# Optimization experiments

Hardware: AMD Instinct MI355X
Metric: run time of the kernel (lower is better)

## Reference

```python
import jax, jax.numpy as jnp
import numpy as np

N_HEADS = 16
EMBED = 1024
SEQ = 2048
BATCH = 4
GELU_C = 0.044715
EPS = 1e-5


def gelu_tanh(x):
    return 0.5 * x * (1.0 + jnp.tanh(jnp.sqrt(2.0 / jnp.pi) * (x + GELU_C * x ** 3)))


def layer_norm(x, scale, shift):
    mean = jnp.mean(x, axis=-1, keepdims=True)
    var = jnp.var(x, axis=-1, keepdims=True)
    return scale * (x - mean) / jnp.sqrt(var + EPS) + shift


def setup_inputs() -> dict:
    key = jax.random.key(0)
    ks = jax.random.split(key, 8)
    d = EMBED
    s = 0.02
    return {
        "X": jax.random.normal(ks[0], (BATCH, SEQ, d), dtype=jnp.float32),
        "Wq": jax.random.normal(ks[1], (d, d), dtype=jnp.float32) * s,
        "Wk": jax.random.normal(ks[2], (d, d), dtype=jnp.float32) * s,
        "Wv": jax.random.normal(ks[3], (d, d), dtype=jnp.float32) * s,
        "Wo": jax.random.normal(ks[4], (d, d), dtype=jnp.float32) * s,
        "W1": jax.random.normal(ks[5], (d, 4 * d), dtype=jnp.float32) * s,
        "b1": jnp.zeros((4 * d,), dtype=jnp.float32),
        "W2": jax.random.normal(ks[6], (4 * d, d), dtype=jnp.float32) * s,
        "b2": jnp.zeros((d,), dtype=jnp.float32),
        "ln1_scale": jnp.ones((d,), dtype=jnp.float32),
        "ln1_shift": jnp.zeros((d,), dtype=jnp.float32),
        "ln2_scale": jnp.ones((d,), dtype=jnp.float32),
        "ln2_shift": jnp.zeros((d,), dtype=jnp.float32),
    }


def attention(x, Wq, Wk, Wv, Wo):
    b, s, d = x.shape
    h, dh = N_HEADS, d // N_HEADS
    q = (x @ Wq).reshape(b, s, h, dh).transpose(0, 2, 1, 3)  # [b,h,s,dh]
    k = (x @ Wk).reshape(b, s, h, dh).transpose(0, 2, 1, 3)
    v = (x @ Wv).reshape(b, s, h, dh).transpose(0, 2, 1, 3)
    scores = jnp.einsum("bhqd,bhkd->bhqk", q, k) / jnp.sqrt(jnp.float32(dh))
    causal = jnp.tril(jnp.ones((s, s), dtype=bool))
    scores = jnp.where(causal, scores, -jnp.inf)
    w = jax.nn.softmax(scores, axis=-1)  # dropout rate 0 -> identity
    ctx = jnp.einsum("bhqk,bhkd->bhqd", w, v)
    ctx = ctx.transpose(0, 2, 1, 3).reshape(b, s, d)
    return ctx @ Wo


def reference(X, Wq, Wk, Wv, Wo, W1, b1, W2, b2,
              ln1_scale, ln1_shift, ln2_scale, ln2_shift):
    h = layer_norm(X, ln1_scale, ln1_shift)
    X = X + attention(h, Wq, Wk, Wv, Wo)
    h = layer_norm(X, ln2_scale, ln2_shift)
    h = gelu_tanh(h @ W1 + b1) @ W2 + b2
    return X + h
```

## Files before the change

### kernel.cpp

```cpp
#include <hip/hip_runtime.h>

typedef unsigned short u16;
typedef __attribute__((ext_vector_type(8))) short bf16x8;
typedef __attribute__((ext_vector_type(4))) float fx4;

#define MFMA16(a, b, c) __builtin_amdgcn_mfma_f32_16x16x32_bf16((a), (b), (c), 0, 0, 0)

__device__ __forceinline__ u16 f2bf(float f) {
  unsigned u = __float_as_uint(f);
  u += 0x7fffu + ((u >> 16) & 1u);
  return (u16)(u >> 16);
}

__device__ __forceinline__ void gload_lds16(const void* g, void* l) {
  __builtin_amdgcn_global_load_lds((const __attribute__((address_space(1))) void*)g,
                                   (__attribute__((address_space(3))) void*)l,
                                   16, 0, 0);
}

struct WP {
  const float* s[6];
  u16* d[6];
};
__global__ __launch_bounds__(256) void tcvt_all(WP p) {
  __shared__ float t[32][33];
  const int id = blockIdx.x;
  int which, bx, by, R, C;
  if (id < 4096) {
    which = id >> 10;
    const int q = id & 1023;
    bx = q >> 5; by = q & 31; R = 1024; C = 1024;
  } else if (id < 8192) {
    which = 4;
    const int q = id - 4096;
    bx = q & 127; by = q >> 7; R = 1024; C = 4096;
  } else {
    which = 5;
    const int q = id - 8192;
    bx = q & 31; by = q >> 5; R = 4096; C = 1024;
  }
  const float* src = p.s[which];
  u16* dst = p.d[which];
  const int tx = threadIdx.x & 31, ty = threadIdx.x >> 5;
#pragma unroll
  for (int i = 0; i < 4; ++i)
    t[ty + i * 8][tx] = src[(size_t)(by * 32 + ty + i * 8) * C + bx * 32 + tx];
  __syncthreads();
#pragma unroll
  for (int i = 0; i < 4; ++i)
    dst[(size_t)(bx * 32 + ty + i * 8) * R + by * 32 + tx] = f2bf(t[tx][ty + i * 8]);
}

__global__ __launch_bounds__(256) void ln_kernel(const float* __restrict__ x,
                                                 const float* __restrict__ sc,
                                                 const float* __restrict__ sh,
                                                 u16* __restrict__ out) {
  const int row = blockIdx.x, tid = threadIdx.x;
  const float4 v = ((const float4*)(x + (size_t)row * 1024))[tid];
  float s = v.x + v.y + v.z + v.w;
  float ss = v.x * v.x + v.y * v.y + v.z * v.z + v.w * v.w;
#pragma unroll
  for (int d = 32; d >= 1; d >>= 1) {
    s += __shfl_xor(s, d);
    ss += __shfl_xor(ss, d);
  }
  __shared__ float rs[4], rq[4];
  const int w = tid >> 6;
  if ((tid & 63) == 0) { rs[w] = s; rq[w] = ss; }
  __syncthreads();
  s = rs[0] + rs[1] + rs[2] + rs[3];
  ss = rq[0] + rq[1] + rq[2] + rq[3];
  const float mean = s * (1.f / 1024.f);
  const float var = ss * (1.f / 1024.f) - mean * mean;
  const float rstd = rsqrtf(var + 1e-5f);
  const float4 g = ((const float4*)sc)[tid];
  const float4 b = ((const float4*)sh)[tid];
  ushort4 o;
  o.x = f2bf(g.x * (v.x - mean) * rstd + b.x);
  o.y = f2bf(g.y * (v.y - mean) * rstd + b.y);
  o.z = f2bf(g.z * (v.z - mean) * rstd + b.z);
  o.w = f2bf(g.w * (v.w - mean) * rstd + b.w);
  ((ushort4*)(out + (size_t)row * 1024))[tid] = o;
}

__device__ __forceinline__ void xcd_map(int bid, int NTN, int& tMi, int& tNi) {
  const int xcd = bid & 7, i = bid >> 3;
  tMi = xcd + 8 * (i / NTN);
  tNi = i % NTN;
}

template <int MODE, int BN>
__global__ __launch_bounds__(512, 1) void gemm8p(
    const u16* __restrict__ A, const u16* __restrict__ Bt, int K, int NTN,
    void* __restrict__ outp, const float* __restrict__ aux,
    u16* __restrict__ qd, u16* __restrict__ kd, u16* __restrict__ vd) {
  constexpr int WN = (BN == 256) ? 4 : 2;
  constexpr int WM = 8 / WN;
  constexpr int MR = 256 / (16 * WM);
  constexpr int MR2 = MR / 2;
  constexpr int BLOADS = BN / 128;
  __shared__ u16 lA[2][2][256 * 32];
  __shared__ u16 lB[2][2][BN * 32];
  const int tid = threadIdx.x;
  const int lane = tid & 63, w = tid >> 6;
  const int lo = lane & 15, hi = lane >> 4;
  const int wm = w / WN, wn = w % WN;
  int tMi, tNi;
  xcd_map(blockIdx.x, NTN, tMi, tNi);
  const int tM = tMi * 256, tN = tNi * BN;
  const int NT = K >> 6;
  const int NIT = K >> 7;

#define STG_A(TI, KSH, GK)                                                       \
  do {                                                                           \
    _Pragma("unroll") for (int j = 0; j < 2; ++j) {                              \
      const int idx = j * 512 + tid;                                             \
      const int row = idx >> 2, u = idx & 3;                                     \
      gload_lds16(A + (size_t)(tM + row) * K + (GK) + ((u ^ ((row >> 1) & 3)) * 8), \
                  &lA[TI][KSH][idx * 8]);                                        \
    }                                                                            \
  } while (0)
#define STG_B(TI, KSH, GK)                                                       \
  do {                                                                           \
    _Pragma("unroll") for (int j = 0; j < BLOADS; ++j) {                         \
      const int idx = j * 512 + tid;                                             \
      const int row = idx >> 2, u = idx & 3;                                     \
      gload_lds16(Bt + (size_t)(tN + row) * K + (GK) + ((u ^ ((row >> 1) & 3)) * 8), \
                  &lB[TI][KSH][idx * 8]);                                        \
    }                                                                            \
  } while (0)
#define VMW                                                                      \
  do {                                                                           \
    if constexpr (BN == 256) asm volatile("s_waitcnt vmcnt(4)" ::: "memory");    \
    else asm volatile("s_waitcnt vmcnt(3)" ::: "memory");                        \
  } while (0)
#define NOPS ((void)0)

#define PHASE(P, STAGE_STMT, VM)                                                 \
  {                                                                              \
    constexpr int ksg = (P) >> 1;                                                \
    constexpr int mh = (P) & 1;                                                  \
    constexpr int ti = ksg >> 1;                                                 \
    constexpr int ksh = ksg & 1;                                                 \
    bf16x8 afr[MR2];                                                             \
    _Pragma("unroll") for (int mi = 0; mi < MR2; ++mi) {                         \
      const int R = wm * (MR * 16) + (mh * MR2 + mi) * 16 + lo;                  \
      afr[mi] =                                                                  \
          *(const bf16x8*)&lA[ti][ksh][R * 32 + ((hi ^ ((R >> 1) & 3)) * 8)];    \
    }                                                                            \
    if constexpr (mh == 0) {                                                     \
      _Pragma("unroll") for (int n = 0; n < 4; ++n) {                            \
        const int R = wn * 64 + n * 16 + lo;                                     \
        bfr[n] =                                                                 \
            *(const bf16x8*)&lB[ti][ksh][R * 32 + ((hi ^ ((R >> 1) & 3)) * 8)];  \
      }                                                                          \
    }                                                                            \
    STAGE_STMT;                                                                  \
    VM;                                                                          \
    __builtin_amdgcn_s_barrier();                                                \
    asm volatile("s_waitcnt lgkmcnt(0)" ::: "memory");                           \
    __builtin_amdgcn_sched_barrier(0);                                           \
    __builtin_amdgcn_s_setprio(1);                                               \
    _Pragma("unroll") for (int mi = 0; mi < MR2; ++mi)                           \
      _Pragma("unroll") for (int n = 0; n < 4; ++n)                              \
        acc[mh * MR2 + mi][n] = MFMA16(afr[mi], bfr[n], acc[mh * MR2 + mi][n]);  \
    __builtin_amdgcn_s_setprio(0);                                               \
    __builtin_amdgcn_sched_barrier(0);                                           \
    __builtin_amdgcn_s_barrier();                                                \
    __builtin_amdgcn_sched_barrier(0);                                           \
  }

  fx4 acc[MR][4];
#pragma unroll
  for (int m = 0; m < MR; ++m)
#pragma unroll
    for (int n = 0; n < 4; ++n) acc[m][n] = (fx4){0.f, 0.f, 0.f, 0.f};
  bf16x8 bfr[4];

  STG_A(0, 0, 0);
  STG_B(0, 0, 0);
  STG_A(0, 1, 32);
  STG_B(0, 1, 32);
  STG_A(1, 0, 64);
  STG_B(1, 0, 64);
  if constexpr (BN == 256) asm volatile("s_waitcnt vmcnt(4)" ::: "memory");
  else asm volatile("s_waitcnt vmcnt(3)" ::: "memory");
  __builtin_amdgcn_s_barrier();
  __builtin_amdgcn_sched_barrier(0);

  for (int it = 0; it < NIT; ++it) {
    const int t0 = 2 * it;
    const bool g2 = (t0 + 2) < NT, g3 = (t0 + 3) < NT;
    PHASE(0, STG_A(1, 1, (t0 + 1) * 64 + 32), NOPS)
    PHASE(1, STG_B(1, 1, (t0 + 1) * 64 + 32), NOPS)
    PHASE(2, if (g2) STG_A(0, 0, (t0 + 2) * 64), NOPS)
    PHASE(3, if (g2) STG_B(0, 0, (t0 + 2) * 64), VMW)
    PHASE(4, if (g2) STG_A(0, 1, (t0 + 2) * 64 + 32), NOPS)
    PHASE(5, if (g2) STG_B(0, 1, (t0 + 2) * 64 + 32), NOPS)
    PHASE(6, if (g3) STG_A(1, 0, (t0 + 3) * 64), NOPS)
    PHASE(7, if (g3) STG_B(1, 0, (t0 + 3) * 64), VMW)
  }
#undef PHASE
#undef STG_A
#undef STG_B
#undef VMW
#undef NOPS

#pragma unroll
  for (int m = 0; m < MR; ++m) {
    const int rgb = tM + wm * (MR * 16) + m * 16 + hi * 4;
#pragma unroll
    for (int n = 0; n < 4; ++n) {
      const int cg = tN + wn * 64 + n * 16 + lo;
#pragma unroll
      for (int r = 0; r < 4; ++r) {
        const float v = acc[m][n][r];
        const int rg = rgb + r;
        if constexpr (MODE == 0) {
          const int which = cg >> 10, c = cg & 1023;
          const int head = c >> 6, dhi = c & 63;
          const int b = rg >> 11, sidx = rg & 2047;
          const int bh = b * 16 + head;
          const u16 bv = f2bf(v);
          if (which == 0)      qd[((size_t)bh * 2048 + sidx) * 64 + dhi] = bv;
          else if (which == 1) kd[((size_t)bh * 2048 + sidx) * 64 + dhi] = bv;
          else                 vd[((size_t)bh * 64 + dhi) * 2048 + sidx] = bv;
        } else if constexpr (MODE == 1) {
          float* o = (float*)outp;
          const size_t idx = (size_t)rg * 1024 + cg;
          o[idx] = aux[idx] + v;
        } else if constexpr (MODE == 2) {
          const float xx = v + aux[cg];
          const float t2 = xx + 0.044715f * xx * xx * xx;
          const float e = __expf(1.5957691216057308f * t2);
          const float th = 1.f - 2.f / (e + 1.f);
          ((u16*)outp)[(size_t)rg * 4096 + cg] = f2bf(0.5f * xx * (1.f + th));
        } else {
          float* o = (float*)outp;
          const size_t idx = (size_t)rg * 1024 + cg;
          o[idx] = o[idx] + v + aux[cg];
        }
      }
    }
  }
}

__global__ __launch_bounds__(512) void attn_kernel(const u16* __restrict__ Q,
                                                   const u16* __restrict__ Kg,
                                                   const u16* __restrict__ Vt,
                                                   u16* __restrict__ ctx) {
  __shared__ u16 lK[2][64 * 64];
  __shared__ u16 lV[2][64 * 64];
  __shared__ u16 Plds[8][16 * 64];
  const int tid = threadIdx.x;
  const int w = tid >> 6, lane = tid & 63;
  const int lo = lane & 15, hi = lane >> 4;
  const int bh = blockIdx.x;
  const int j = blockIdx.y;
  const u16* Qb = Q + (size_t)bh * 2048 * 64;
  const u16* Kb = Kg + (size_t)bh * 2048 * 64;
  const u16* Vb = Vt + (size_t)bh * 64 * 2048;
  u16* Pw = Plds[w];
  const int nt0 = 2 * j + 2;

  const int rowS = tid >> 3;
  const int ugS = (tid & 7) ^ (rowS & 7);

#define STAGE(BUF, KB)                                                         \
  do {                                                                         \
    gload_lds16(Kb + (size_t)((KB) + rowS) * 64 + ugS * 8, &lK[BUF][tid * 8]); \
    gload_lds16(Vb + (size_t)rowS * 2048 + (KB) + ugS * 8, &lV[BUF][tid * 8]); \
  } while (0)

  const int b = bh >> 4, h = bh & 15;
  const float SCALE = 0.18033688011112042f;

  bf16x8 ones;
#pragma unroll
  for (int i = 0; i < 8; ++i) ones[i] = (short)0x3F80;

  int qt = j;
  int qw = qt * 128 + w * 16;

  bf16x8 qf[2];
#pragma unroll
  for (int kc = 0; kc < 2; ++kc)
    qf[kc] = *(const bf16x8*)&Qb[(size_t)(qw + lo) * 64 + kc * 32 + hi * 8];

  fx4 accO[4];
  fx4 accS = (fx4){0.f, 0.f, 0.f, 0.f};
#pragma unroll
  for (int t2 = 0; t2 < 4; ++t2) accO[t2] = (fx4){0.f, 0.f, 0.f, 0.f};

  STAGE(0, 0);
  __syncthreads();

  int buf = 0;
  for (int t = 0; t < 34; ++t) {
    if (t + 1 < 34) {
      const int tn = t + 1;
      const int kbn = (tn < nt0 ? tn : tn - nt0) * 64;
      STAGE(buf ^ 1, kbn);
    }
    if (t == nt0) {
#pragma unroll
      for (int t2 = 0; t2 < 4; ++t2)
#pragma unroll
        for (int r = 0; r < 4; ++r) {
          const int rg = b * 2048 + qw + hi * 4 + r;
          const int cg = h * 64 + t2 * 16 + lo;
          ctx[(size_t)rg * 1024 + cg] = f2bf(accO[t2][r] / accS[r]);
        }
      qt = 15 - j;
      qw = qt * 128 + w * 16;
#pragma unroll
      for (int kc = 0; kc < 2; ++kc)
        qf[kc] = *(const bf16x8*)&Qb[(size_t)(qw + lo) * 64 + kc * 32 + hi * 8];
#pragma unroll
      for (int t2 = 0; t2 < 4; ++t2) accO[t2] = (fx4){0.f, 0.f, 0.f, 0.f};
      accS = (fx4){0.f, 0.f, 0.f, 0.f};
    }
    const int kb = (t < nt0 ? t : t - nt0) * 64;
    if (kb <= qw + 15) {
      const u16* lKb = lK[buf];
      const u16* lVb = lV[buf];
      fx4 s[4];
#pragma unroll
      for (int tt = 0; tt < 4; ++tt) {
        const int r = tt * 16 + lo;
        const bf16x8 kf0 = *(const bf16x8*)&lKb[r * 64 + ((hi ^ (r & 7)) << 3)];
        const bf16x8 kf1 = *(const bf16x8*)&lKb[r * 64 + (((4 + hi) ^ (r & 7)) << 3)];
        fx4 z = (fx4){0.f, 0.f, 0.f, 0.f};
        z = MFMA16(qf[0], kf0, z);
        z = MFMA16(qf[1], kf1, z);
        s[tt] = z;
      }
      if (kb + 63 > qw) {
#pragma unroll
        for (int tt = 0; tt < 4; ++tt)
#pragma unroll
          for (int r = 0; r < 4; ++r) {
            const int key = kb + tt * 16 + lo;
            const int qr = qw + hi * 4 + r;
            s[tt][r] = (key > qr) ? 0.f : exp2f(s[tt][r] * SCALE);
          }
      } else {
#pragma unroll
        for (int tt = 0; tt < 4; ++tt)
#pragma unroll
          for (int r = 0; r < 4; ++r) s[tt][r] = exp2f(s[tt][r] * SCALE);
      }
#pragma unroll
      for (int r = 0; r < 4; ++r) {
        unsigned pk01, pk23;
        asm("v_cvt_pk_bf16_f32 %0, %1, %2" : "=v"(pk01) : "v"(s[0][r]), "v"(s[1][r]));
        asm("v_cvt_pk_bf16_f32 %0, %1, %2" : "=v"(pk23) : "v"(s[2][r]), "v"(s[3][r]));
        const int row = hi * 4 + r;
        const int sw = (row & 7) << 4;
        const int rbase = row * 128;
        Pw[(rbase + (((0 * 16 + lo) * 2) ^ sw)) >> 1] = (u16)pk01;
        Pw[(rbase + (((1 * 16 + lo) * 2) ^ sw)) >> 1] = (u16)(pk01 >> 16);
        Pw[(rbase + (((2 * 16 + lo) * 2) ^ sw)) >> 1] = (u16)pk23;
        Pw[(rbase + (((3 * 16 + lo) * 2) ^ sw)) >> 1] = (u16)(pk23 >> 16);
      }
      asm volatile("s_waitcnt lgkmcnt(0)" ::: "memory");
      bf16x8 pf[2];
#pragma unroll
      for (int kc = 0; kc < 2; ++kc) {
        const int row = lo;
        const int colB = kc * 64 + hi * 16;
        pf[kc] = *(const bf16x8*)((const char*)Pw + row * 128 + (colB ^ ((row & 7) << 4)));
      }
      accS = MFMA16(pf[0], ones, accS);
      accS = MFMA16(pf[1], ones, accS);
#pragma unroll
      for (int t2 = 0; t2 < 4; ++t2) {
        const int r2 = t2 * 16 + lo;
        const bf16x8 vf0 = *(const bf16x8*)&lVb[r2 * 64 + ((hi ^ (r2 & 7)) << 3)];
        const bf16x8 vf1 = *(const bf16x8*)&lVb[r2 * 64 + (((4 + hi) ^ (r2 & 7)) << 3)];
        accO[t2] = MFMA16(pf[0], vf0, accO[t2]);
        accO[t2] = MFMA16(pf[1], vf1, accO[t2]);
      }
    }
    __syncthreads();
    buf ^= 1;
  }
#pragma unroll
  for (int t2 = 0; t2 < 4; ++t2)
#pragma unroll
    for (int r = 0; r < 4; ++r) {
      const int rg = b * 2048 + qw + hi * 4 + r;
      const int cg = h * 64 + t2 * 16 + lo;
      ctx[(size_t)rg * 1024 + cg] = f2bf(accO[t2][r] / accS[r]);
    }
#undef STAGE
}

extern "C" void kernel_launch(void* const* d_in, const int* in_sizes, int n_in,
                              void* d_out, int out_size, void* d_ws, size_t ws_size,
                              hipStream_t stream) {
  const float* X    = (const float*)d_in[0];
  const float* Wq   = (const float*)d_in[1];
  const float* Wk   = (const float*)d_in[2];
  const float* Wv   = (const float*)d_in[3];
  const float* Wo   = (const float*)d_in[4];
  const float* W1   = (const float*)d_in[5];
  const float* b1   = (const float*)d_in[6];
  const float* W2   = (const float*)d_in[7];
  const float* b2   = (const float*)d_in[8];
  const float* ln1s = (const float*)d_in[9];
  const float* ln1b = (const float*)d_in[10];
  const float* ln2s = (const float*)d_in[11];
  const float* ln2b = (const float*)d_in[12];

  const size_t SZ_WQKVT = 3072UL * 1024;
  const size_t SZ_WOT   = 1024UL * 1024;
  const size_t SZ_W1T   = 4096UL * 1024;
  const size_t SZ_W2T   = 1024UL * 4096;
  const size_t SZ_H     = 8192UL * 1024;
  const size_t SZ_QKV   = 64UL * 2048 * 64;

  u16* WqkvT = (u16*)d_ws;
  u16* WoT   = WqkvT + SZ_WQKVT;
  u16* W1T   = WoT + SZ_WOT;
  u16* W2T   = W1T + SZ_W1T;
  u16* hbuf  = W2T + SZ_W2T;
  u16* qbuf  = hbuf + SZ_H;
  u16* kbuf  = qbuf + SZ_QKV;
  u16* vbuf  = kbuf + SZ_QKV;
  u16* gbuf  = vbuf + SZ_QKV;
  u16* ctx   = hbuf;
  u16* h2    = qbuf;

  float* out = (float*)d_out;
  dim3 blk(256);

  WP wp;
  wp.s[0] = Wq; wp.s[1] = Wk; wp.s[2] = Wv; wp.s[3] = Wo; wp.s[4] = W1; wp.s[5] = W2;
  wp.d[0] = WqkvT;
  wp.d[1] = WqkvT + 1024 * 1024;
  wp.d[2] = WqkvT + 2 * 1024 * 1024;
  wp.d[3] = WoT;
  wp.d[4] = W1T;
  wp.d[5] = W2T;
  tcvt_all<<<12288, blk, 0, stream>>>(wp);

  ln_kernel<<<8192, blk, 0, stream>>>(X, ln1s, ln1b, hbuf);
  gemm8p<0, 128><<<768, dim3(512), 0, stream>>>(hbuf, WqkvT, 1024, 24,
                                                nullptr, nullptr, qbuf, kbuf, vbuf);
  attn_kernel<<<dim3(64, 8), dim3(512), 0, stream>>>(qbuf, kbuf, vbuf, ctx);
  gemm8p<1, 128><<<256, dim3(512), 0, stream>>>(ctx, WoT, 1024, 8,
                                                out, X, nullptr, nullptr, nullptr);
  ln_kernel<<<8192, blk, 0, stream>>>(out, ln2s, ln2b, h2);
  gemm8p<2, 256><<<512, dim3(512), 0, stream>>>(h2, W1T, 1024, 16,
                                                gbuf, b1, nullptr, nullptr, nullptr);
  gemm8p<3, 128><<<256, dim3(512), 0, stream>>>(gbuf, W2T, 4096, 8,
                                                out, b2, nullptr, nullptr, nullptr);
}
```

Baseline: 414.2 us.

## Add four-phase GEMM pipeline for 256x128 tiles with peeled final iteration

Adds a separate GEMM kernel for the 256x128 tile case. Each phase loads all A and B fragments for one 32-wide k-slice and issues one combined A+B stage, giving four phases per two k-tiles instead of eight. The last iteration is peeled so it needs no conditional loads, and its vmcnt waits are tuned to drain the queue. The QKV, output-projection and W2 GEMMs now use this kernel, while W1 keeps the 8-phase 256x256 kernel. The change aims to cut barrier and phase overhead, at the cost of fewer MFMAs per phase to hide load latency and more registers held for fragments.

```diff
diff --git a/kernel.cpp b/kernel.cpp
--- a/kernel.cpp
+++ b/kernel.cpp
@@ -89,132 +89,17 @@
   tNi = i % NTN;
 }
 
-template <int MODE, int BN>
-__global__ __launch_bounds__(512, 1) void gemm8p(
-    const u16* __restrict__ A, const u16* __restrict__ Bt, int K, int NTN,
-    void* __restrict__ outp, const float* __restrict__ aux,
-    u16* __restrict__ qd, u16* __restrict__ kd, u16* __restrict__ vd) {
-  constexpr int WN = (BN == 256) ? 4 : 2;
-  constexpr int WM = 8 / WN;
-  constexpr int MR = 256 / (16 * WM);
-  constexpr int MR2 = MR / 2;
-  constexpr int BLOADS = BN / 128;
-  __shared__ u16 lA[2][2][256 * 32];
-  __shared__ u16 lB[2][2][BN * 32];
-  const int tid = threadIdx.x;
-  const int lane = tid & 63, w = tid >> 6;
-  const int lo = lane & 15, hi = lane >> 4;
-  const int wm = w / WN, wn = w % WN;
-  int tMi, tNi;
-  xcd_map(blockIdx.x, NTN, tMi, tNi);
-  const int tM = tMi * 256, tN = tNi * BN;
-  const int NT = K >> 6;
-  const int NIT = K >> 7;
-
-#define STG_A(TI, KSH, GK)                                                       \
-  do {                                                                           \
-    _Pragma("unroll") for (int j = 0; j < 2; ++j) {                              \
-      const int idx = j * 512 + tid;                                             \
-      const int row = idx >> 2, u = idx & 3;                                     \
-      gload_lds16(A + (size_t)(tM + row) * K + (GK) + ((u ^ ((row >> 1) & 3)) * 8), \
-                  &lA[TI][KSH][idx * 8]);                                        \
-    }                                                                            \
-  } while (0)
-#define STG_B(TI, KSH, GK)                                                       \
-  do {                                                                           \
-    _Pragma("unroll") for (int j = 0; j < BLOADS; ++j) {                         \
-      const int idx = j * 512 + tid;                                             \
-      const int row = idx >> 2, u = idx & 3;                                     \
-      gload_lds16(Bt + (size_t)(tN + row) * K + (GK) + ((u ^ ((row >> 1) & 3)) * 8), \
-                  &lB[TI][KSH][idx * 8]);                                        \
-    }                                                                            \
-  } while (0)
-#define VMW                                                                      \
-  do {                                                                           \
-    if constexpr (BN == 256) asm volatile("s_waitcnt vmcnt(4)" ::: "memory");    \
-    else asm volatile("s_waitcnt vmcnt(3)" ::: "memory");                        \
-  } while (0)
-#define NOPS ((void)0)
-
-#define PHASE(P, STAGE_STMT, VM)                                                 \
-  {                                                                              \
-    constexpr int ksg = (P) >> 1;                                                \
-    constexpr int mh = (P) & 1;                                                  \
-    constexpr int ti = ksg >> 1;                                                 \
-    constexpr int ksh = ksg & 1;                                                 \
-    bf16x8 afr[MR2];                                                             \
-    _Pragma("unroll") for (int mi = 0; mi < MR2; ++mi) {                         \
-      const int R = wm * (MR * 16) + (mh * MR2 + mi) * 16 + lo;                  \
-      afr[mi] =                                                                  \
-          *(const bf16x8*)&lA[ti][ksh][R * 32 + ((hi ^ ((R >> 1) & 3)) * 8)];    \
-    }                                                                            \
-    if constexpr (mh == 0) {                                                     \
-      _Pragma("unroll") for (int n = 0; n < 4; ++n) {                            \
-        const int R = wn * 64 + n * 16 + lo;                                     \
-        bfr[n] =                                                                 \
-            *(const bf16x8*)&lB[ti][ksh][R * 32 + ((hi ^ ((R >> 1) & 3)) * 8)];  \
-      }                                                                          \
-    }                                                                            \
-    STAGE_STMT;                                                                  \
-    VM;                                                                          \
-    __builtin_amdgcn_s_barrier();                                                \
-    asm volatile("s_waitcnt lgkmcnt(0)" ::: "memory");                           \
-    __builtin_amdgcn_sched_barrier(0);                                           \
-    __builtin_amdgcn_s_setprio(1);                                               \
-    _Pragma("unroll") for (int mi = 0; mi < MR2; ++mi)                           \
-      _Pragma("unroll") for (int n = 0; n < 4; ++n)                              \
-        acc[mh * MR2 + mi][n] = MFMA16(afr[mi], bfr[n], acc[mh * MR2 + mi][n]);  \
-    __builtin_amdgcn_s_setprio(0);                                               \
-    __builtin_amdgcn_sched_barrier(0);                                           \
-    __builtin_amdgcn_s_barrier();                                                \
-    __builtin_amdgcn_sched_barrier(0);                                           \
-  }
-
-  fx4 acc[MR][4];
-#pragma unroll
-  for (int m = 0; m < MR; ++m)
-#pragma unroll
-    for (int n = 0; n < 4; ++n) acc[m][n] = (fx4){0.f, 0.f, 0.f, 0.f};
-  bf16x8 bfr[4];
-
-  STG_A(0, 0, 0);
-  STG_B(0, 0, 0);
-  STG_A(0, 1, 32);
-  STG_B(0, 1, 32);
-  STG_A(1, 0, 64);
-  STG_B(1, 0, 64);
-  if constexpr (BN == 256) asm volatile("s_waitcnt vmcnt(4)" ::: "memory");
-  else asm volatile("s_waitcnt vmcnt(3)" ::: "memory");
-  __builtin_amdgcn_s_barrier();
-  __builtin_amdgcn_sched_barrier(0);
-
-  for (int it = 0; it < NIT; ++it) {
-    const int t0 = 2 * it;
-    const bool g2 = (t0 + 2) < NT, g3 = (t0 + 3) < NT;
-    PHASE(0, STG_A(1, 1, (t0 + 1) * 64 + 32), NOPS)
-    PHASE(1, STG_B(1, 1, (t0 + 1) * 64 + 32), NOPS)
-    PHASE(2, if (g2) STG_A(0, 0, (t0 + 2) * 64), NOPS)
-    PHASE(3, if (g2) STG_B(0, 0, (t0 + 2) * 64), VMW)
-    PHASE(4, if (g2) STG_A(0, 1, (t0 + 2) * 64 + 32), NOPS)
-    PHASE(5, if (g2) STG_B(0, 1, (t0 + 2) * 64 + 32), NOPS)
-    PHASE(6, if (g3) STG_A(1, 0, (t0 + 3) * 64), NOPS)
-    PHASE(7, if (g3) STG_B(1, 0, (t0 + 3) * 64), VMW)
-  }
-#undef PHASE
-#undef STG_A
-#undef STG_B
-#undef VMW
-#undef NOPS
-
-#pragma unroll
+template <int MODE>
+__device__ __forceinline__ void gemm_epilogue(const fx4* acc4, int MR, int tM, int tN,
+                                              int wm, int wn, int lo, int hi,
+                                              void* outp, const float* aux,
+                                              u16* qd, u16* kd, u16* vd) {
   for (int m = 0; m < MR; ++m) {
     const int rgb = tM + wm * (MR * 16) + m * 16 + hi * 4;
-#pragma unroll
     for (int n = 0; n < 4; ++n) {
       const int cg = tN + wn * 64 + n * 16 + lo;
-#pragma unroll
       for (int r = 0; r < 4; ++r) {
-        const float v = acc[m][n][r];
+        const float v = acc4[m * 4 + n][r];
         const int rg = rgb + r;
         if constexpr (MODE == 0) {
           const int which = cg >> 10, c = cg & 1023;
@@ -245,6 +130,208 @@
   }
 }
 
+template <int MODE>
+__global__ __launch_bounds__(512, 1) void gemm4p(
+    const u16* __restrict__ A, const u16* __restrict__ Bt, int K, int NTN,
+    void* __restrict__ outp, const float* __restrict__ aux,
+    u16* __restrict__ qd, u16* __restrict__ kd, u16* __restrict__ vd) {
+  __shared__ u16 lA[2][2][256 * 32];
+  __shared__ u16 lB[2][2][128 * 32];
+  const int tid = threadIdx.x;
+  const int lane = tid & 63, w = tid >> 6;
+  const int lo = lane & 15, hi = lane >> 4;
+  const int wm = w >> 1, wn = w & 1;
+  int tMi, tNi;
+  xcd_map(blockIdx.x, NTN, tMi, tNi);
+  const int tM = tMi * 256, tN = tNi * 128;
+  const int NT = K >> 6;
+  const int NIT = K >> 7;
+
+#define STG4(TI, H, GK)                                                           \
+  do {                                                                            \
+    _Pragma("unroll") for (int j = 0; j < 2; ++j) {                               \
+      const int idx = j * 512 + tid;                                              \
+      const int row = idx >> 2, u = idx & 3;                                      \
+      gload_lds16(A + (size_t)(tM + row) * K + (GK) + ((u ^ ((row >> 1) & 3)) * 8), \
+                  &lA[TI][H][idx * 8]);                                           \
+    }                                                                             \
+    {                                                                             \
+      const int row = tid >> 2, u = tid & 3;                                      \
+      gload_lds16(Bt + (size_t)(tN + row) * K + (GK) + ((u ^ ((row >> 1) & 3)) * 8), \
+                  &lB[TI][H][tid * 8]);                                           \
+    }                                                                             \
+  } while (0)
+
+#define PHASE4(TI, H, STAGE_STMT, VMSTR)                                          \
+  {                                                                               \
+    bf16x8 afr[4], bfr[4];                                                        \
+    _Pragma("unroll") for (int mi = 0; mi < 4; ++mi) {                            \
+      const int R = wm * 64 + mi * 16 + lo;                                       \
+      afr[mi] = *(const bf16x8*)&lA[TI][H][R * 32 + ((hi ^ ((R >> 1) & 3)) * 8)]; \
+    }                                                                             \
+    _Pragma("unroll") for (int n = 0; n < 4; ++n) {                               \
+      const int R = wn * 64 + n * 16 + lo;                                        \
+      bfr[n] = *(const bf16x8*)&lB[TI][H][R * 32 + ((hi ^ ((R >> 1) & 3)) * 8)];  \
+    }                                                                             \
+    STAGE_STMT;                                                                   \
+    asm volatile("s_waitcnt " VMSTR ::: "memory");                                \
+    __builtin_amdgcn_s_barrier();                                                 \
+    asm volatile("s_waitcnt lgkmcnt(0)" ::: "memory");                            \
+    __builtin_amdgcn_sched_barrier(0);                                            \
+    __builtin_amdgcn_s_setprio(1);                                                \
+    _Pragma("unroll") for (int mi = 0; mi < 4; ++mi)                              \
+      _Pragma("unroll") for (int n = 0; n < 4; ++n)                               \
+        acc[mi][n] = MFMA16(afr[mi], bfr[n], acc[mi][n]);                         \
+    __builtin_amdgcn_s_setprio(0);                                                \
+    __builtin_amdgcn_sched_barrier(0);                                            \
+    __builtin_amdgcn_s_barrier();                                                 \
+    __builtin_amdgcn_sched_barrier(0);                                            \
+  }
+
+  fx4 acc[4][4];
+#pragma unroll
+  for (int m = 0; m < 4; ++m)
+#pragma unroll
+    for (int n = 0; n < 4; ++n) acc[m][n] = (fx4){0.f, 0.f, 0.f, 0.f};
+
+  STG4(0, 0, 0);
+  STG4(0, 1, 32);
+  STG4(1, 0, 64);
+  asm volatile("s_waitcnt vmcnt(6)" ::: "memory");
+  __builtin_amdgcn_s_barrier();
+  __builtin_amdgcn_sched_barrier(0);
+
+  for (int it = 0; it < NIT - 1; ++it) {
+    const int t0 = 2 * it;
+    PHASE4(0, 0, STG4(1, 1, (t0 + 1) * 64 + 32), "vmcnt(6)")
+    PHASE4(0, 1, STG4(0, 0, (t0 + 2) * 64), "vmcnt(6)")
+    PHASE4(1, 0, STG4(0, 1, (t0 + 2) * 64 + 32), "vmcnt(6)")
+    PHASE4(1, 1, STG4(1, 0, (t0 + 3) * 64), "vmcnt(6)")
+  }
+  {
+    const int t0 = NT - 2;
+    PHASE4(0, 0, STG4(1, 1, (t0 + 1) * 64 + 32), "vmcnt(6)")
+    PHASE4(0, 1, ((void)0), "vmcnt(3)")
+    PHASE4(1, 0, ((void)0), "vmcnt(0)")
+    PHASE4(1, 1, ((void)0), "vmcnt(0)")
+  }
+#undef PHASE4
+#undef STG4
+
+  gemm_epilogue<MODE>(&acc[0][0], 4, tM, tN, wm, wn, lo, hi, outp, aux, qd, kd, vd);
+}
+
+template <int MODE>
+__global__ __launch_bounds__(512, 1) void gemm8p(
+    const u16* __restrict__ A, const u16* __restrict__ Bt, int K, int NTN,
+    void* __restrict__ outp, const float* __restrict__ aux,
+    u16* __restrict__ qd, u16* __restrict__ kd, u16* __restrict__ vd) {
+  constexpr int MR = 8, MR2 = 4;
+  __shared__ u16 lA[2][2][256 * 32];
+  __shared__ u16 lB[2][2][256 * 32];
+  const int tid = threadIdx.x;
+  const int lane = tid & 63, w = tid >> 6;
+  const int lo = lane & 15, hi = lane >> 4;
+  const int wm = w >> 2, wn = w & 3;
+  int tMi, tNi;
+  xcd_map(blockIdx.x, NTN, tMi, tNi);
+  const int tM = tMi * 256, tN = tNi * 256;
+  const int NT = K >> 6;
+  const int NIT = K >> 7;
+
+#define STG_A(TI, KSH, GK)                                                        \
+  do {                                                                            \
+    _Pragma("unroll") for (int j = 0; j < 2; ++j) {                               \
+      const int idx = j * 512 + tid;                                              \
+      const int row = idx >> 2, u = idx & 3;                                      \
+      gload_lds16(A + (size_t)(tM + row) * K + (GK) + ((u ^ ((row >> 1) & 3)) * 8), \
+                  &lA[TI][KSH][idx * 8]);                                         \
+    }                                                                             \
+  } while (0)
+#define STG_B(TI, KSH, GK)                                                        \
+  do {                                                                            \
+    _Pragma("unroll") for (int j = 0; j < 2; ++j) {                               \
+      const int idx = j * 512 + tid;                                              \
+      const int row = idx >> 2, u = idx & 3;                                      \
+      gload_lds16(Bt + (size_t)(tN + row) * K + (GK) + ((u ^ ((row >> 1) & 3)) * 8), \
+                  &lB[TI][KSH][idx * 8]);                                         \
+    }                                                                             \
+  } while (0)
+#define VMW asm volatile("s_waitcnt vmcnt(4)" ::: "memory")
+#define NOPS ((void)0)
+
+#define PHASE(P, STAGE_STMT, VM)                                                  \
+  {                                                                               \
+    constexpr int ksg = (P) >> 1;                                                 \
+    constexpr int mh = (P) & 1;                                                   \
+    constexpr int ti = ksg >> 1;                                                  \
+    constexpr int ksh = ksg & 1;                                                  \
+    bf16x8 afr[MR2];                                                              \
+    _Pragma("unroll") for (int mi = 0; mi < MR2; ++mi) {                          \
+      const int R = wm * (MR * 16) + (mh * MR2 + mi) * 16 + lo;                   \
+      afr[mi] =                                                                   \
+          *(const bf16x8*)&lA[ti][ksh][R * 32 + ((hi ^ ((R >> 1) & 3)) * 8)];     \
+    }                                                                             \
+    if constexpr (mh == 0) {                                                      \
+      _Pragma("unroll") for (int n = 0; n < 4; ++n) {                             \
+        const int R = wn * 64 + n * 16 + lo;                                      \
+        bfr[n] =                                                                  \
+            *(const bf16x8*)&lB[ti][ksh][R * 32 + ((hi ^ ((R >> 1) & 3)) * 8)];   \
+      }                                                                           \
+    }                                                                             \
+    STAGE_STMT;                                                                   \
+    VM;                                                                           \
+    __builtin_amdgcn_s_barrier();                                                 \
+    asm volatile("s_waitcnt lgkmcnt(0)" ::: "memory");                            \
+    __builtin_amdgcn_sched_barrier(0);                                            \
+    __builtin_amdgcn_s_setprio(1);                                                \
+    _Pragma("unroll") for (int mi = 0; mi < MR2; ++mi)                            \
+      _Pragma("unroll") for (int n = 0; n < 4; ++n)                               \
+        acc[mh * MR2 + mi][n] = MFMA16(afr[mi], bfr[n], acc[mh * MR2 + mi][n]);   \
+    __builtin_amdgcn_s_setprio(0);                                                \
+    __builtin_amdgcn_sched_barrier(0);                                            \
+    __builtin_amdgcn_s_barrier();                                                 \
+    __builtin_amdgcn_sched_barrier(0);                                            \
+  }
+
+  fx4 acc[MR][4];
+#pragma unroll
+  for (int m = 0; m < MR; ++m)
+#pragma unroll
+    for (int n = 0; n < 4; ++n) acc[m][n] = (fx4){0.f, 0.f, 0.f, 0.f};
+  bf16x8 bfr[4];
+
+  STG_A(0, 0, 0);
+  STG_B(0, 0, 0);
+  STG_A(0, 1, 32);
+  STG_B(0, 1, 32);
+  STG_A(1, 0, 64);
+  STG_B(1, 0, 64);
+  asm volatile("s_waitcnt vmcnt(4)" ::: "memory");
+  __builtin_amdgcn_s_barrier();
+  __builtin_amdgcn_sched_barrier(0);
+
+  for (int it = 0; it < NIT; ++it) {
+    const int t0 = 2 * it;
+    const bool g2 = (t0 + 2) < NT, g3 = (t0 + 3) < NT;
+    PHASE(0, STG_A(1, 1, (t0 + 1) * 64 + 32), NOPS)
+    PHASE(1, STG_B(1, 1, (t0 + 1) * 64 + 32), NOPS)
+    PHASE(2, if (g2) STG_A(0, 0, (t0 + 2) * 64), NOPS)
+    PHASE(3, if (g2) STG_B(0, 0, (t0 + 2) * 64), VMW)
+    PHASE(4, if (g2) STG_A(0, 1, (t0 + 2) * 64 + 32), NOPS)
+    PHASE(5, if (g2) STG_B(0, 1, (t0 + 2) * 64 + 32), NOPS)
+    PHASE(6, if (g3) STG_A(1, 0, (t0 + 3) * 64), NOPS)
+    PHASE(7, if (g3) STG_B(1, 0, (t0 + 3) * 64), VMW)
+  }
+#undef PHASE
+#undef STG_A
+#undef STG_B
+#undef VMW
+#undef NOPS
+
+  gemm_epilogue<MODE>(&acc[0][0], MR, tM, tN, wm, wn, lo, hi, outp, aux, qd, kd, vd);
+}
+
 __global__ __launch_bounds__(512) void attn_kernel(const u16* __restrict__ Q,
                                                    const u16* __restrict__ Kg,
                                                    const u16* __restrict__ Vt,
@@ -446,14 +533,14 @@
   tcvt_all<<<12288, blk, 0, stream>>>(wp);
 
   ln_kernel<<<8192, blk, 0, stream>>>(X, ln1s, ln1b, hbuf);
-  gemm8p<0, 128><<<768, dim3(512), 0, stream>>>(hbuf, WqkvT, 1024, 24,
-                                                nullptr, nullptr, qbuf, kbuf, vbuf);
+  gemm4p<0><<<768, dim3(512), 0, stream>>>(hbuf, WqkvT, 1024, 24,
+                                           nullptr, nullptr, qbuf, kbuf, vbuf);
   attn_kernel<<<dim3(64, 8), dim3(512), 0, stream>>>(qbuf, kbuf, vbuf, ctx);
-  gemm8p<1, 128><<<256, dim3(512), 0, stream>>>(ctx, WoT, 1024, 8,
-                                                out, X, nullptr, nullptr, nullptr);
+  gemm4p<1><<<256, dim3(512), 0, stream>>>(ctx, WoT, 1024, 8,
+                                           out, X, nullptr, nullptr, nullptr);
   ln_kernel<<<8192, blk, 0, stream>>>(out, ln2s, ln2b, h2);
-  gemm8p<2, 256><<<512, dim3(512), 0, stream>>>(h2, W1T, 1024, 16,
-                                                gbuf, b1, nullptr, nullptr, nullptr);
-  gemm8p<3, 128><<<256, dim3(512), 0, stream>>>(gbuf, W2T, 4096, 8,
-                                                out, b2, nullptr, nullptr, nullptr);
-}
+  gemm8p<2><<<512, dim3(512), 0, stream>>>(h2, W1T, 1024, 16,
+                                           gbuf, b1, nullptr, nullptr, nullptr);
+  gemm4p<3><<<256, dim3(512), 0, stream>>>(gbuf, W2T, 4096, 8,
+                                           out, b2, nullptr, nullptr, nullptr);
+}
```

New measurement: 996.4 us. 141% more time.
